# Performance work log

Hardware: AMD Instinct MI355X
Metric: run time of the kernel (lower is better)

The kernel has to match this reference:

```python
import jax, jax.numpy as jnp
import numpy as np

HID = 256   # hidden_dim
P = 16      # pool_size
EPS = 1e-5


def _ln(x, g, b):
    m = x.mean(-1, keepdims=True)
    v = x.var(-1, keepdims=True)
    return (x - m) * jax.lax.rsqrt(v + EPS) * g + b


def setup_inputs() -> dict:
    key = jax.random.key(0)
    ks = jax.random.split(key, 12)
    B, Cf, H, W = 8, 512, 64, 64
    Cg = Cf // 2
    Co = Cf // 2
    s = 0.02
    d = {}
    d['e_f'] = jax.random.normal(ks[0], (B, Cf, H, W), jnp.float32)
    d['e_g'] = jax.random.normal(ks[1], (B, Cg, H, W), jnp.float32)
    d['l_feat'] = jax.random.normal(ks[2], (B, 768, 20), jnp.float32)
    d['l_mask'] = jnp.ones((B, 20, 1), jnp.float32)
    d['ln_f_g'] = jnp.ones((Cf,), jnp.float32)
    d['ln_f_b'] = jnp.zeros((Cf,), jnp.float32)
    d['ln_g_g'] = jnp.ones((Cg,), jnp.float32)
    d['ln_g_b'] = jnp.zeros((Cg,), jnp.float32)
    d['wq'] = jax.random.normal(ks[3], (Cf, HID), jnp.float32) * s
    d['bq'] = jnp.zeros((HID,), jnp.float32)
    d['wk'] = jax.random.normal(ks[4], (Cg, HID), jnp.float32) * s
    d['bk'] = jnp.zeros((HID,), jnp.float32)
    d['wv'] = jax.random.normal(ks[5], (Cg, HID), jnp.float32) * s
    d['bv'] = jnp.zeros((HID,), jnp.float32)
    d['wo'] = jax.random.normal(ks[6], (HID, HID), jnp.float32) * s
    d['bo'] = jnp.zeros((HID,), jnp.float32)
    d['dw_k'] = jax.random.normal(ks[7], (HID, 1, 3, 3), jnp.float32) * s  # depthwise kernel (OIHW, I=1)
    d['efp_w'] = jax.random.normal(ks[8], (HID, Cf), jnp.float32) * s     # 1x1 conv v_channels->hidden
    d['efp_b'] = jnp.zeros((HID,), jnp.float32)
    d['outc_w'] = jax.random.normal(ks[9], (Co, HID), jnp.float32) * s    # 1x1 conv hidden->out
    d['outc_b'] = jnp.zeros((Co,), jnp.float32)
    d['bn_g'] = jnp.ones((Co,), jnp.float32)
    d['bn_b'] = jnp.zeros((Co,), jnp.float32)
    d['bn_m'] = jnp.zeros((Co,), jnp.float32)
    d['bn_v'] = jnp.ones((Co,), jnp.float32)
    return d


def reference(e_f, e_g, l_feat, l_mask, ln_f_g, ln_f_b, ln_g_g, ln_g_b,
              wq, bq, wk, bk, wv, bv, wo, bo, dw_k, efp_w, efp_b,
              outc_w, outc_b, bn_g, bn_b, bn_m, bn_v):
    B, Cf, H, W = e_f.shape
    # Q = w_qi(LN(e_f))                                  (B, HW, HID)
    q = _ln(e_f.transpose(0, 2, 3, 1), ln_f_g, ln_f_b).reshape(B, H * W, Cf) @ wq + bq
    # K/V projections from LN(e_g)
    g = _ln(e_g.transpose(0, 2, 3, 1), ln_g_g, ln_g_b).reshape(B, H * W, -1)
    k = (g @ wk + bk).reshape(B, H, W, HID)
    v = (g @ wv + bv).reshape(B, H, W, HID)
    # 16x16 max/avg pooling -> (B, Hp*Wp, HID)
    k = jnp.max(k.reshape(B, H // P, P, W // P, P, HID), axis=(2, 4)).reshape(B, -1, HID)
    v = jnp.mean(v.reshape(B, H // P, P, W // P, P, HID), axis=(2, 4)).reshape(B, -1, HID)
    # pooled attention
    attn = jax.nn.softmax(jnp.einsum('bqd,bkd->bqk', q, k) * (HID ** -0.5), axis=-1)
    a_i = jnp.einsum('bqk,bkd->bqd', attn, v)  # (B, HW, HID)
    # depthwise 3x3 conv on Q (NCHW)
    q_nchw = q.reshape(B, H, W, HID).transpose(0, 3, 1, 2)
    dw = jax.lax.conv_general_dilated(q_nchw, dw_k, (1, 1), [(1, 1), (1, 1)],
                                      feature_group_count=HID)
    combined = dw + a_i.reshape(B, H, W, HID).transpose(0, 3, 1, 2)
    comb = combined.transpose(0, 2, 3, 1).reshape(B, H * W, HID) @ wo + bo
    comb = comb.reshape(B, H, W, HID).transpose(0, 3, 1, 2)
    # 1x1 proj of e_f, elementwise gate
    efp = jnp.einsum('bchw,oc->bohw', e_f, efp_w) + efp_b[None, :, None, None]
    e_a = efp * comb
    # out: 1x1 conv + BN (inference) + ReLU (dropout inactive in eval)
    out = jnp.einsum('bchw,oc->bohw', e_a, outc_w) + outc_b[None, :, None, None]
    scale = (bn_g * jax.lax.rsqrt(bn_v + EPS))[None, :, None, None]
    out = (out - bn_m[None, :, None, None]) * scale + bn_b[None, :, None, None]
    return jax.nn.relu(out)
```

## Files before the change

### kernel.cpp

```cpp
#include <hip/hip_runtime.h>
#include <math.h>

#define EPS 1e-5f

typedef __attribute__((ext_vector_type(8))) short bf16x8;
typedef __attribute__((ext_vector_type(4))) float f32x4;

__device__ __forceinline__ unsigned short f2bf(float f) {
    unsigned int u = __float_as_uint(f);
    u += 0x7fff + ((u >> 16) & 1);
    return (unsigned short)(u >> 16);
}
__device__ __forceinline__ float bf2f(unsigned short h) {
    return __uint_as_float(((unsigned int)h) << 16);
}
__device__ __forceinline__ float lof(unsigned int u) {
    return __uint_as_float(u << 16);
}
__device__ __forceinline__ float hif(unsigned int u) {
    return __uint_as_float(u & 0xffff0000u);
}
__device__ __forceinline__ void async16(void* lds, const void* g) {
    __builtin_amdgcn_global_load_lds(
        (const __attribute__((address_space(1))) unsigned int*)g,
        (__attribute__((address_space(3))) unsigned int*)lds, 16, 0, 0);
}

__global__ __launch_bounds__(256) void trans_prep(
    const float* __restrict__ ef, const float* __restrict__ eg,
    unsigned short* __restrict__ ef_bf, unsigned short* __restrict__ eg_bf,
    float* __restrict__ pf, float* __restrict__ pfq,
    float* __restrict__ pg, float* __restrict__ pgq,
    const float* __restrict__ lnfg, const float* __restrict__ lnfb,
    const float* __restrict__ wq, const float* __restrict__ bq,
    const float* __restrict__ efpw, const float* __restrict__ efpb,
    const float* __restrict__ lngg, const float* __restrict__ lngb,
    const float* __restrict__ wk, const float* __restrict__ bk,
    const float* __restrict__ wv, const float* __restrict__ bv,
    const float* __restrict__ wo, const float* __restrict__ outcw,
    const float* __restrict__ outcb, const float* __restrict__ bng,
    const float* __restrict__ bnb, const float* __restrict__ bnm,
    const float* __restrict__ bnv, const float* __restrict__ dwk,
    unsigned short* __restrict__ Wb1t, unsigned short* __restrict__ Wb2t,
    unsigned short* __restrict__ Wot, unsigned short* __restrict__ Woc,
    float* __restrict__ dwt,
    float* __restrict__ cs1, float* __restrict__ cst1,
    float* __restrict__ cs2, float* __restrict__ cst2,
    float* __restrict__ scv, float* __restrict__ shv)
{
    __shared__ float tile[64][65];
    __shared__ float psum[4][64], pss[4][64];
    int id = blockIdx.x;
    int t = threadIdx.x;
    if (id < 3072) {
        const float* src; unsigned short* dst; float* ps; float* pq;
        int C, cblk, b, p0;
        if (id < 2048) {
            src = ef; dst = ef_bf; ps = pf; pq = pfq; C = 512;
            b = id >> 8; cblk = (id >> 5) & 7; p0 = (id & 31) * 128;
        } else {
            id -= 2048;
            src = eg; dst = eg_bf; ps = pg; pq = pgq; C = 256;
            b = id >> 7; cblk = (id >> 5) & 3; p0 = (id & 31) * 128;
        }
        int c0 = cblk * 64;
        const float* s = src + ((size_t)b * C + c0) * 4096 + p0;
        int cr = t >> 4, p4 = (t & 15) * 4;
        int lane = t & 63, grp = t >> 6;
        int pr = t >> 3, c8 = (t & 7) * 8;

        float4 r1[4], r2[4];
#pragma unroll
        for (int i = 0; i < 4; i++)
            r1[i] = *(const float4*)(s + (size_t)(i * 16 + cr) * 4096 + p4);
#pragma unroll
        for (int i = 0; i < 4; i++)
            r2[i] = *(const float4*)(s + (size_t)(i * 16 + cr) * 4096 + 64 + p4);

#pragma unroll
        for (int half = 0; half < 2; half++) {
#pragma unroll
            for (int i = 0; i < 4; i++) {
                float4 v = half ? r2[i] : r1[i];
                int c = i * 16 + cr;
                tile[c][p4 + 0] = v.x; tile[c][p4 + 1] = v.y;
                tile[c][p4 + 2] = v.z; tile[c][p4 + 3] = v.w;
            }
            __syncthreads();

            int pbase = p0 + half * 64;
            unsigned short* d = dst + ((size_t)(b * 4096 + pbase)) * C + c0;
#pragma unroll
            for (int i = 0; i < 2; i++) {
                int p = i * 32 + pr;
                uint4 pk;
                pk.x = (unsigned)f2bf(tile[c8 + 0][p]) | ((unsigned)f2bf(tile[c8 + 1][p]) << 16);
                pk.y = (unsigned)f2bf(tile[c8 + 2][p]) | ((unsigned)f2bf(tile[c8 + 3][p]) << 16);
                pk.z = (unsigned)f2bf(tile[c8 + 4][p]) | ((unsigned)f2bf(tile[c8 + 5][p]) << 16);
                pk.w = (unsigned)f2bf(tile[c8 + 6][p]) | ((unsigned)f2bf(tile[c8 + 7][p]) << 16);
                *(uint4*)(d + (size_t)p * C + c8) = pk;
            }

            float sm = 0.f, sq = 0.f;
#pragma unroll
            for (int j = 0; j < 16; j++) {
                float v = tile[grp * 16 + j][lane];
                sm += v; sq += v * v;
            }
            psum[grp][lane] = sm; pss[grp][lane] = sq;
            __syncthreads();
            if (t < 64) {
                float fs = psum[0][t] + psum[1][t] + psum[2][t] + psum[3][t];
                float fq = pss[0][t] + pss[1][t] + pss[2][t] + pss[3][t];
                ps[cblk * 32768 + b * 4096 + pbase + t] = fs;
                pq[cblk * 32768 + b * 4096 + pbase + t] = fq;
            }
            if (half == 0) __syncthreads();
        }
    } else {
        int id2 = id - 3072;
        float* red1 = (float*)psum;
        float* red2 = (float*)pss;
        if (id2 < 64) {
            const float* src; unsigned short* dst; const float* scale;
            int K, k0, n0;
            if (id2 < 32) {
                src = wq; dst = Wb1t; scale = lnfg; K = 512;
                k0 = (id2 >> 2) * 64; n0 = (id2 & 3) * 64;
            } else if (id2 < 48) {
                int j = id2 - 32;
                src = wk; dst = Wb2t; scale = lngg; K = 256;
                k0 = (j >> 2) * 64; n0 = (j & 3) * 64;
            } else {
                int j = id2 - 48;
                src = wo; dst = Wot; scale = nullptr; K = 256;
                k0 = (j >> 2) * 64; n0 = (j & 3) * 64;
            }
            int rr = t >> 6, cc = t & 63;
#pragma unroll
            for (int i = 0; i < 16; i++) {
                int r = i * 4 + rr;
                tile[r][cc] = src[(size_t)(k0 + r) * 256 + n0 + cc];
            }
            __syncthreads();
            int nn = t >> 3, k8 = (t & 7) * 8;
#pragma unroll
            for (int i = 0; i < 2; i++) {
                int n = i * 32 + nn;
                float v[8];
#pragma unroll
                for (int j = 0; j < 8; j++) {
                    float s = scale ? scale[k0 + k8 + j] : 1.f;
                    v[j] = s * tile[k8 + j][n];
                }
                uint4 pk;
                pk.x = (unsigned)f2bf(v[0]) | ((unsigned)f2bf(v[1]) << 16);
                pk.y = (unsigned)f2bf(v[2]) | ((unsigned)f2bf(v[3]) << 16);
                pk.z = (unsigned)f2bf(v[4]) | ((unsigned)f2bf(v[5]) << 16);
                pk.w = (unsigned)f2bf(v[6]) | ((unsigned)f2bf(v[7]) << 16);
                *(uint4*)(dst + (size_t)(n0 + n) * K + k0 + k8) = pk;
            }
        } else if (id2 < 192) {
            int j = (id2 - 64) * 1024 + t * 4;
            float4 v = *(const float4*)(efpw + j);
            uint2 pk;
            pk.x = (unsigned)f2bf(v.x) | ((unsigned)f2bf(v.y) << 16);
            pk.y = (unsigned)f2bf(v.z) | ((unsigned)f2bf(v.w) << 16);
            *(uint2*)(Wb1t + 131072 + j) = pk;
        } else if (id2 < 256) {
            int j = (id2 - 192) * 1024 + t * 4;
            float4 v = *(const float4*)(outcw + j);
            uint2 pk;
            pk.x = (unsigned)f2bf(v.x) | ((unsigned)f2bf(v.y) << 16);
            pk.y = (unsigned)f2bf(v.z) | ((unsigned)f2bf(v.w) << 16);
            *(uint2*)(Woc + j) = pk;
        } else if (id2 == 256) {
#pragma unroll
            for (int tap = 0; tap < 9; tap++)
                dwt[tap * 256 + t] = dwk[t * 9 + tap];
        } else if (id2 < 265) {
            int n0 = (id2 - 257) * 32;
            int nl = t & 31, kq = t >> 5;
            float cs = 0.f, ct = 0.f;
#pragma unroll 4
            for (int kk = 0; kk < 64; kk++) {
                int k = kq * 64 + kk;
                float w = wq[k * 256 + n0 + nl];
                cs += lnfg[k] * w; ct += lnfb[k] * w;
            }
            red1[kq * 32 + nl] = cs; red2[kq * 32 + nl] = ct;
            __syncthreads();
            if (t < 32) {
                float s = 0.f, c2 = 0.f;
#pragma unroll
                for (int q = 0; q < 8; q++) { s += red1[q * 32 + t]; c2 += red2[q * 32 + t]; }
                int n = n0 + t;
                cs1[n] = s; cst1[n] = c2 + bq[n];
                cs1[256 + n] = 0.f; cst1[256 + n] = efpb[n];
            }
        } else if (id2 < 273) {
            int n0 = (id2 - 265) * 32;
            int nl = t & 31, kq = t >> 5;
            float cs = 0.f, ct = 0.f;
#pragma unroll 4
            for (int kk = 0; kk < 32; kk++) {
                int k = kq * 32 + kk;
                float w = wk[k * 256 + n0 + nl];
                cs += lngg[k] * w; ct += lngb[k] * w;
            }
            red1[kq * 32 + nl] = cs; red2[kq * 32 + nl] = ct;
            __syncthreads();
            if (t < 32) {
                float s = 0.f, c2 = 0.f;
#pragma unroll
                for (int q = 0; q < 8; q++) { s += red1[q * 32 + t]; c2 += red2[q * 32 + t]; }
                int n = n0 + t;
                cs2[n] = s; cst2[n] = c2 + bk[n];
            }
        } else if (id2 < 281) {
            int n0 = (id2 - 273) * 32;
            int nl = t & 31, kq = t >> 5;
            float cs = 0.f, ct = 0.f;
#pragma unroll 4
            for (int kk = 0; kk < 32; kk++) {
                int k = kq * 32 + kk;
                float w = wv[k * 256 + n0 + nl];
                cs += lngg[k] * w; ct += lngb[k] * w;
            }
            red1[kq * 32 + nl] = cs; red2[kq * 32 + nl] = ct;
            __syncthreads();
            if (t < 32) {
                float s = 0.f, c2 = 0.f;
#pragma unroll
                for (int q = 0; q < 8; q++) { s += red1[q * 32 + t]; c2 += red2[q * 32 + t]; }
                int n = n0 + t;
                cs2[256 + n] = s; cst2[256 + n] = c2 + bv[n];
            }
        } else {
            int n = t;
            float s = bng[n] * rsqrtf(bnv[n] + EPS);
            scv[n] = s;
            shv[n] = (outcb[n] - bnm[n]) * s + bnb[n];
        }
    }
}

template<int K>
__device__ __forceinline__ void mfma_core(
    const unsigned short* __restrict__ A, const unsigned short* __restrict__ Bt,
    int m0, int n0, unsigned short* As, unsigned short* Bs, f32x4 acc[4][4])
{
    const int tid = threadIdx.x;
    const int wave = tid >> 6, lane = tid & 63;
    const int wm = (wave & 1) * 64, wn = (wave >> 1) * 64;
#pragma unroll
    for (int i = 0; i < 4; i++)
#pragma unroll
        for (int j = 0; j < 4; j++) acc[i][j] = (f32x4){0.f, 0.f, 0.f, 0.f};

    const int srow = wave * 32 + (lane >> 3);
    const int sg = (lane & 7) ^ ((lane >> 3) & 7);
    const unsigned short* ga = A + (size_t)(m0 + srow) * K + sg * 8;
    const unsigned short* gb = Bt + (size_t)(n0 + srow) * K + sg * 8;

    for (int k0 = 0; k0 < K; k0 += 64) {
#pragma unroll
        for (int t = 0; t < 4; t++) {
            async16(As + (wave * 32 + t * 8) * 64, ga + (size_t)t * 8 * K + k0);
            async16(Bs + (wave * 32 + t * 8) * 64, gb + (size_t)t * 8 * K + k0);
        }
        __syncthreads();
#pragma unroll
        for (int ks = 0; ks < 2; ks++) {
            bf16x8 af[4], bfr[4];
            int kb = ks * 4 + (lane >> 4);
            int slot = (kb ^ (lane & 7)) * 8;
#pragma unroll
            for (int i = 0; i < 4; i++) {
                int m = wm + i * 16 + (lane & 15);
                af[i] = *(const bf16x8*)&As[m * 64 + slot];
                int n = wn + i * 16 + (lane & 15);
                bfr[i] = *(const bf16x8*)&Bs[n * 64 + slot];
            }
#pragma unroll
            for (int i = 0; i < 4; i++)
#pragma unroll
                for (int j = 0; j < 4; j++)
                    acc[i][j] = __builtin_amdgcn_mfma_f32_16x16x32_bf16(
                        af[i], bfr[j], acc[i][j], 0, 0, 0);
        }
        __syncthreads();
    }
}

__global__ __launch_bounds__(256, 2) void gemm_proj(
    const unsigned short* __restrict__ ef_bf, const unsigned short* __restrict__ Wb1t,
    const float* __restrict__ cs1, const float* __restrict__ cst1,
    const float* __restrict__ pf, const float* __restrict__ pfq,
    unsigned short* __restrict__ qbuf, unsigned short* __restrict__ efpbuf,
    const unsigned short* __restrict__ eg_bf, const unsigned short* __restrict__ Wb2t,
    const float* __restrict__ cs2, const float* __restrict__ cst2,
    const float* __restrict__ pg, const float* __restrict__ pgq,
    float* __restrict__ mg, float* __restrict__ rg,
    unsigned short* __restrict__ kfull)
{
    __shared__ unsigned short As[128 * 64];
    __shared__ unsigned short Bs[256 * 64];
    __shared__ float sstat[256];
    const int tid = threadIdx.x;
    const int wave = tid >> 6, lane = tid & 63;
    const int bid = blockIdx.x;

    if (bid < 512) {
        const int m0 = (bid >> 1) * 128, n0 = (bid & 1) * 256;
        const int wm = (wave & 1) * 64, wn = (wave >> 1) * 128;
        f32x4 acc[4][8];

        if (tid < 128) {
            int gm = m0 + tid;
            float s = 0.f, q = 0.f;
#pragma unroll
            for (int i = 0; i < 8; i++) { s += pf[i * 32768 + gm]; q += pfq[i * 32768 + gm]; }
            float m = s * (1.f / 512.f);
            sstat[tid] = m;
            sstat[128 + tid] = rsqrtf(q * (1.f / 512.f) - m * m + EPS);
        }

#pragma unroll
        for (int i = 0; i < 4; i++)
#pragma unroll
            for (int j = 0; j < 8; j++) acc[i][j] = (f32x4){0.f, 0.f, 0.f, 0.f};

        const int srow = lane >> 3;
        const int sg = (lane & 7) ^ (srow & 7);
        const unsigned short* ga = ef_bf + (size_t)(m0 + wave * 32 + srow) * 512 + sg * 8;
        const unsigned short* gb = Wb1t + (size_t)(n0 + wave * 64 + srow) * 512 + sg * 8;

        for (int k0 = 0; k0 < 512; k0 += 64) {
#pragma unroll
            for (int t = 0; t < 4; t++)
                async16(As + (wave * 32 + t * 8) * 64, ga + (size_t)t * 8 * 512 + k0);
#pragma unroll
            for (int t = 0; t < 8; t++)
                async16(Bs + (wave * 64 + t * 8) * 64, gb + (size_t)t * 8 * 512 + k0);
            __syncthreads();
#pragma unroll
            for (int ks = 0; ks < 2; ks++) {
                bf16x8 af[4], bfr[8];
                int kb = ks * 4 + (lane >> 4);
                int slot = (kb ^ (lane & 7)) * 8;
#pragma unroll
                for (int i = 0; i < 4; i++)
                    af[i] = *(const bf16x8*)&As[(wm + i * 16 + (lane & 15)) * 64 + slot];
#pragma unroll
                for (int j = 0; j < 8; j++)
                    bfr[j] = *(const bf16x8*)&Bs[(wn + j * 16 + (lane & 15)) * 64 + slot];
#pragma unroll
                for (int i = 0; i < 4; i++)
#pragma unroll
                    for (int j = 0; j < 8; j++)
                        acc[i][j] = __builtin_amdgcn_mfma_f32_16x16x32_bf16(
                            af[i], bfr[j], acc[i][j], 0, 0, 0);
            }
            __syncthreads();
        }

        bool isq = (n0 == 0);
#pragma unroll
        for (int i = 0; i < 4; i++) {
#pragma unroll
            for (int r = 0; r < 4; r++) {
                int lm = wm + i * 16 + ((lane >> 4) * 4) + r;
                int gm = m0 + lm;
                float mean = sstat[lm], rs = sstat[128 + lm];
#pragma unroll
                for (int j = 0; j < 8; j++) {
                    int nn = wn + j * 16 + (lane & 15);
                    float v = acc[i][j][r];
                    if (isq) {
                        int n = nn;
                        float o = rs * (v - mean * cs1[n]) + cst1[n];
                        qbuf[(size_t)gm * 256 + nn] = f2bf(o);
                    } else {
                        int n = nn + 256;
                        efpbuf[(size_t)gm * 256 + nn] = f2bf(v + cst1[n]);
                    }
                }
            }
        }
    } else {
        const int j2 = bid - 512;
        const int m0 = (j2 >> 1) * 128, n0 = (j2 & 1) * 128;
        f32x4 acc[4][4];

        if (tid < 128) {
            int gm = m0 + tid;
            float s = 0.f, q = 0.f;
#pragma unroll
            for (int i = 0; i < 4; i++) { s += pg[i * 32768 + gm]; q += pgq[i * 32768 + gm]; }
            float m = s * (1.f / 256.f);
            float r = rsqrtf(q * (1.f / 256.f) - m * m + EPS);
            sstat[tid] = m; sstat[128 + tid] = r;
            if (n0 == 0) { mg[gm] = m; rg[gm] = r; }
        }

        mfma_core<256>(eg_bf, Wb2t, m0, n0, As, Bs, acc);
        int wm = (wave & 1) * 64, wn = (wave >> 1) * 64;
#pragma unroll
        for (int i = 0; i < 4; i++) {
#pragma unroll
            for (int r = 0; r < 4; r++) {
                int lm = wm + i * 16 + ((lane >> 4) * 4) + r;
                int gm = m0 + lm;
                float mean = sstat[lm], rs = sstat[128 + lm];
#pragma unroll
                for (int j = 0; j < 4; j++) {
                    int n = n0 + wn + j * 16 + (lane & 15);
                    float o = rs * (acc[i][j][r] - mean * cs2[n]) + cst2[n];
                    kfull[(size_t)gm * 256 + n] = f2bf(o);
                }
            }
        }
    }
}

__global__ __launch_bounds__(256) void pool_phase(
    const unsigned short* __restrict__ kfull, const float* __restrict__ eg,
    const float* __restrict__ rg, const float* __restrict__ mg,
    unsigned short* __restrict__ kpb, float* __restrict__ s1,
    float* __restrict__ s0)
{
    __shared__ float smem[4352];
    int id = blockIdx.x;
    int t = threadIdx.x;
    if (id < 128) {
        int b = id >> 4, cell = id & 15;
        int hp = cell >> 2, wp = cell & 3;
        int g8 = t & 31, rr = t >> 5;
        float kmx[8];
#pragma unroll
        for (int j = 0; j < 8; j++) kmx[j] = -3.402823466e38f;
#pragma unroll
        for (int rsub = 0; rsub < 2; rsub++) {
            int r = rr * 2 + rsub;
            int prow = (hp * 16 + r) * 64 + wp * 16;
            for (int cl = 0; cl < 16; cl++) {
                size_t basei = ((size_t)(b * 4096 + prow + cl)) * 256 + g8 * 8;
                uint4 kv = *(const uint4*)(kfull + basei);
                kmx[0] = fmaxf(kmx[0], lof(kv.x)); kmx[1] = fmaxf(kmx[1], hif(kv.x));
                kmx[2] = fmaxf(kmx[2], lof(kv.y)); kmx[3] = fmaxf(kmx[3], hif(kv.y));
                kmx[4] = fmaxf(kmx[4], lof(kv.z)); kmx[5] = fmaxf(kmx[5], hif(kv.z));
                kmx[6] = fmaxf(kmx[6], lof(kv.w)); kmx[7] = fmaxf(kmx[7], hif(kv.w));
            }
        }
#pragma unroll
        for (int j = 0; j < 8; j++) smem[rr * 256 + g8 * 8 + j] = kmx[j];
        __syncthreads();
        float m = smem[t];
#pragma unroll
        for (int r2 = 1; r2 < 8; r2++) m = fmaxf(m, smem[r2 * 256 + t]);
        kpb[(size_t)(b * 16 + cell) * 256 + t] = f2bf(m);
    } else {
        int id2 = id - 128;
        int b = id2 >> 6, hp = (id2 >> 4) & 3, cgrp = id2 & 15;
        int rr = t >> 4, cq = t & 15, cx = cq >> 2;
        int p = (hp * 16 + rr) * 64 + cq * 4;
        float4 w4 = *(const float4*)&rg[b * 4096 + p];
        float part[16];
        const float* egb = eg + ((size_t)b * 256 + cgrp * 16) * 4096 + p;
#pragma unroll
        for (int cc = 0; cc < 16; cc++) {
            float4 v4 = *(const float4*)(egb + (size_t)cc * 4096);
            part[cc] = w4.x * v4.x + w4.y * v4.y + w4.z * v4.z + w4.w * v4.w;
        }
#pragma unroll
        for (int cc = 0; cc < 16; cc++) smem[t * 16 + cc] = part[cc];
        if (cgrp == 0) {
            float4 m4 = *(const float4*)&mg[b * 4096 + p];
            smem[4096 + t] = w4.x * m4.x + w4.y * m4.y + w4.z * m4.z + w4.w * m4.w;
        }
        __syncthreads();
        if (t < 64) {
            int cx2 = t >> 4, cc = t & 15;
            float sacc = 0.f;
#pragma unroll
            for (int rr2 = 0; rr2 < 16; rr2++)
#pragma unroll
                for (int dq = 0; dq < 4; dq++)
                    sacc += smem[(rr2 * 16 + cx2 * 4 + dq) * 16 + cc];
            s1[((size_t)(b * 16 + hp * 4 + cx2)) * 256 + cgrp * 16 + cc] = sacc;
        }
        if (cgrp == 0 && t < 4) {
            float sacc = 0.f;
#pragma unroll
            for (int rr2 = 0; rr2 < 16; rr2++)
#pragma unroll
                for (int dq = 0; dq < 4; dq++)
                    sacc += smem[4096 + rr2 * 16 + t * 4 + dq];
            s0[b * 16 + hp * 4 + t] = sacc;
        }
    }
}

__global__ __launch_bounds__(256) void vpool_gemm(
    const float* __restrict__ s1, const float* __restrict__ s0,
    const float* __restrict__ lngg, const float* __restrict__ wv,
    const float* __restrict__ cs2, const float* __restrict__ cst2,
    float* __restrict__ vp)
{
    int cell = blockIdx.x;
    int n = threadIdx.x;
    const float* s1r = s1 + (size_t)cell * 256;
    float acc = 0.f;
    for (int c = 0; c < 256; c++)
        acc = fmaf(lngg[c] * s1r[c], wv[c * 256 + n], acc);
    vp[(size_t)cell * 256 + n] = acc * (1.f / 256.f)
        - (s0[cell] * (1.f / 256.f)) * cs2[256 + n] + cst2[256 + n];
}

__global__ __launch_bounds__(256) void combined_dw(
    const unsigned short* __restrict__ qbuf, const unsigned short* __restrict__ kpb,
    const float* __restrict__ vp, const float* __restrict__ dwt,
    unsigned short* __restrict__ combined)
{
    __shared__ float attns[256];
    int wave = threadIdx.x >> 6, lane = threadIdx.x & 63;
    int id = blockIdx.x;
    int b = id & 7, seg = id >> 3;
    int pidx0 = seg * 16;

    if (wave == 0) {
        int fr = lane & 15, quad = lane >> 4;
        const unsigned short* qrow = qbuf + (size_t)(b * 4096 + pidx0 + fr) * 256 + quad * 8;
        const unsigned short* krow = kpb + (size_t)(b * 16 + fr) * 256 + quad * 8;
        f32x4 sacc = {0.f, 0.f, 0.f, 0.f};
#pragma unroll
        for (int ks = 0; ks < 8; ks++) {
            bf16x8 af = *(const bf16x8*)(qrow + ks * 32);
            bf16x8 bf_ = *(const bf16x8*)(krow + ks * 32);
            sacc = __builtin_amdgcn_mfma_f32_16x16x32_bf16(af, bf_, sacc, 0, 0, 0);
        }
#pragma unroll
        for (int r = 0; r < 4; r++) {
            float s = sacc[r] * 0.0625f;
            float mx = s;
#pragma unroll
            for (int off = 8; off >= 1; off >>= 1) mx = fmaxf(mx, __shfl_xor(mx, off));
            float e = __expf(s - mx);
            float sum = e;
#pragma unroll
            for (int off = 8; off >= 1; off >>= 1) sum += __shfl_xor(sum, off);
            attns[(quad * 4 + r) * 16 + fr] = e / sum;
        }
    }
    __syncthreads();

    int pidx = pidx0 + wave * 4;
    int h = pidx >> 6, w0 = pidx & 63;
    int o4 = lane * 4;

    float4 kreg[9];
#pragma unroll
    for (int tap = 0; tap < 9; tap++)
        kreg[tap] = *(const float4*)&dwt[tap * 256 + o4];

    float4 acc[4];
#pragma unroll
    for (int i = 0; i < 4; i++) acc[i] = (float4){0.f, 0.f, 0.f, 0.f};

    const float* arow = attns + (wave * 4) * 16;
#pragma unroll
    for (int c = 0; c < 16; c++) {
        float4 v = *(const float4*)&vp[(size_t)(b * 16 + c) * 256 + o4];
#pragma unroll
        for (int i = 0; i < 4; i++) {
            float a = arow[i * 16 + c];
            acc[i].x = fmaf(a, v.x, acc[i].x); acc[i].y = fmaf(a, v.y, acc[i].y);
            acc[i].z = fmaf(a, v.z, acc[i].z); acc[i].w = fmaf(a, v.w, acc[i].w);
        }
    }
#pragma unroll
    for (int dy = 0; dy < 3; dy++) {
        int hh = h + dy - 1;
        if (hh < 0 || hh > 63) continue;
        const unsigned short* qr = qbuf + ((size_t)(b * 4096 + hh * 64)) * 256;
        float4 ft[6];
#pragma unroll
        for (int c = 0; c < 6; c++) {
            int xx = w0 - 1 + c;
            if (xx < 0 || xx > 63) {
                ft[c] = (float4){0.f, 0.f, 0.f, 0.f};
            } else {
                uint2 qa = *(const uint2*)(qr + (size_t)xx * 256 + o4);
                ft[c] = (float4){lof(qa.x), hif(qa.x), lof(qa.y), hif(qa.y)};
            }
        }
#pragma unroll
        for (int dx = 0; dx < 3; dx++) {
            float4 kk = kreg[dy * 3 + dx];
#pragma unroll
            for (int i = 0; i < 4; i++) {
                float4 qv = ft[i + dx];
                acc[i].x = fmaf(qv.x, kk.x, acc[i].x);
                acc[i].y = fmaf(qv.y, kk.y, acc[i].y);
                acc[i].z = fmaf(qv.z, kk.z, acc[i].z);
                acc[i].w = fmaf(qv.w, kk.w, acc[i].w);
            }
        }
    }
#pragma unroll
    for (int i = 0; i < 4; i++) {
        uint2 pk;
        pk.x = (unsigned)f2bf(acc[i].x) | ((unsigned)f2bf(acc[i].y) << 16);
        pk.y = (unsigned)f2bf(acc[i].z) | ((unsigned)f2bf(acc[i].w) << 16);
        *(uint2*)(combined + ((size_t)(b * 4096 + pidx + i)) * 256 + o4) = pk;
    }
}

__global__ __launch_bounds__(256) void gemm34_mfma(
    const unsigned short* __restrict__ comb, const unsigned short* __restrict__ Wot,
    const float* __restrict__ bo, const unsigned short* __restrict__ efp,
    const unsigned short* __restrict__ Woc,
    const float* __restrict__ scv, const float* __restrict__ shv,
    float* __restrict__ outp)
{
    __shared__ unsigned short As[64 * 64];
    __shared__ unsigned short Bs[256 * 64];
    __shared__ unsigned short eat[64 * 256];
    const int tid = threadIdx.x;
    const int wave = tid >> 6, lane = tid & 63;
    const int m0 = blockIdx.x * 64;

    const int srow = lane >> 3;
    const int sg = (lane & 7) ^ (srow & 7);

    f32x4 acc[4][4];
#pragma unroll
    for (int i = 0; i < 4; i++)
#pragma unroll
        for (int j = 0; j < 4; j++) acc[i][j] = (f32x4){0.f, 0.f, 0.f, 0.f};

    const unsigned short* ga = comb + (size_t)(m0 + wave * 16 + srow) * 256 + sg * 8;
    const unsigned short* gb = Wot + (size_t)(wave * 64 + srow) * 256 + sg * 8;

    for (int k0 = 0; k0 < 256; k0 += 64) {
#pragma unroll
        for (int t = 0; t < 2; t++)
            async16(As + (wave * 16 + t * 8) * 64, ga + (size_t)t * 8 * 256 + k0);
#pragma unroll
        for (int t = 0; t < 8; t++)
            async16(Bs + (wave * 64 + t * 8) * 64, gb + (size_t)t * 8 * 256 + k0);
        __syncthreads();
#pragma unroll
        for (int ks = 0; ks < 2; ks++) {
            bf16x8 af[4], bfr[4];
            int kb = ks * 4 + (lane >> 4);
            int slot = (kb ^ (lane & 7)) * 8;
#pragma unroll
            for (int i = 0; i < 4; i++) {
                af[i]  = *(const bf16x8*)&As[(i * 16 + (lane & 15)) * 64 + slot];
                bfr[i] = *(const bf16x8*)&Bs[(wave * 64 + i * 16 + (lane & 15)) * 64 + slot];
            }
#pragma unroll
            for (int i = 0; i < 4; i++)
#pragma unroll
                for (int j = 0; j < 4; j++)
                    acc[i][j] = __builtin_amdgcn_mfma_f32_16x16x32_bf16(
                        af[i], bfr[j], acc[i][j], 0, 0, 0);
        }
        __syncthreads();
    }

    float bo4[4];
#pragma unroll
    for (int j = 0; j < 4; j++) bo4[j] = bo[wave * 64 + j * 16 + (lane & 15)];
#pragma unroll
    for (int i = 0; i < 4; i++) {
#pragma unroll
        for (int r = 0; r < 4; r++) {
            int pos = i * 16 + ((lane >> 4) * 4) + r;
#pragma unroll
            for (int j = 0; j < 4; j++) {
                int n = wave * 64 + j * 16 + (lane & 15);
                float o = (acc[i][j][r] + bo4[j])
                          * bf2f(efp[(size_t)(m0 + pos) * 256 + n]);
                int o8 = j * 2 + ((lane >> 3) & 1);
                int slot = o8 ^ (pos & 7);
                eat[pos * 256 + wave * 64 + slot * 8 + (lane & 7)] = f2bf(o);
            }
        }
    }

    f32x4 acc2[4][4];
#pragma unroll
    for (int i = 0; i < 4; i++)
#pragma unroll
        for (int j = 0; j < 4; j++) acc2[i][j] = (f32x4){0.f, 0.f, 0.f, 0.f};

    const unsigned short* gw = Woc + (size_t)(wave * 64 + srow) * 256 + sg * 8;
    for (int k0 = 0; k0 < 256; k0 += 64) {
#pragma unroll
        for (int t = 0; t < 8; t++)
            async16(Bs + (wave * 64 + t * 8) * 64, gw + (size_t)t * 8 * 256 + k0);
        __syncthreads();
        int kc = k0 >> 6;
#pragma unroll
        for (int ks = 0; ks < 2; ks++) {
            bf16x8 af2[4], bf2_[4];
            int kb = ks * 4 + (lane >> 4);
            int slot = (kb ^ (lane & 7)) * 8;
#pragma unroll
            for (int i = 0; i < 4; i++) {
                af2[i]  = *(const bf16x8*)&Bs[(wave * 64 + i * 16 + (lane & 15)) * 64 + slot];
                bf2_[i] = *(const bf16x8*)&eat[(i * 16 + (lane & 15)) * 256 + kc * 64 + slot];
            }
#pragma unroll
            for (int i = 0; i < 4; i++)
#pragma unroll
                for (int j = 0; j < 4; j++)
                    acc2[i][j] = __builtin_amdgcn_mfma_f32_16x16x32_bf16(
                        af2[i], bf2_[j], acc2[i][j], 0, 0, 0);
        }
        __syncthreads();
    }

#pragma unroll
    for (int i = 0; i < 4; i++) {
#pragma unroll
        for (int r = 0; r < 4; r++) {
            int co = wave * 64 + i * 16 + ((lane >> 4) * 4) + r;
            float s = scv[co], hh = shv[co];
#pragma unroll
            for (int j = 0; j < 4; j++) {
                int p = m0 + j * 16 + (lane & 15);
                float o = fmaxf(fmaf(acc2[i][j][r], s, hh), 0.f);
                outp[((size_t)(p >> 12)) * 1048576 + (size_t)co * 4096 + (p & 4095)] = o;
            }
        }
    }
}

extern "C" void kernel_launch(void* const* d_in, const int* in_sizes, int n_in,
                              void* d_out, int out_size, void* d_ws, size_t ws_size,
                              hipStream_t stream)
{
    const float* e_f   = (const float*)d_in[0];
    const float* e_g   = (const float*)d_in[1];
    const float* lnfg  = (const float*)d_in[4];
    const float* lnfb  = (const float*)d_in[5];
    const float* lngg  = (const float*)d_in[6];
    const float* lngb  = (const float*)d_in[7];
    const float* wq    = (const float*)d_in[8];
    const float* bq    = (const float*)d_in[9];
    const float* wk    = (const float*)d_in[10];
    const float* bk    = (const float*)d_in[11];
    const float* wv    = (const float*)d_in[12];
    const float* bv    = (const float*)d_in[13];
    const float* wo    = (const float*)d_in[14];
    const float* bo    = (const float*)d_in[15];
    const float* dwk   = (const float*)d_in[16];
    const float* efpw  = (const float*)d_in[17];
    const float* efpb  = (const float*)d_in[18];
    const float* outcw = (const float*)d_in[19];
    const float* outcb = (const float*)d_in[20];
    const float* bng   = (const float*)d_in[21];
    const float* bnb   = (const float*)d_in[22];
    const float* bnm   = (const float*)d_in[23];
    const float* bnv   = (const float*)d_in[24];
    float* outp = (float*)d_out;

    char* base = (char*)d_ws;
    auto alloc = [&](size_t bytes) -> char* {
        char* r = base; base += (bytes + 255) & ~(size_t)255; return r;
    };
    float* pf    = (float*)alloc(8 * 32768 * 4);
    float* pfq   = (float*)alloc(8 * 32768 * 4);
    float* pg    = (float*)alloc(4 * 32768 * 4);
    float* pgq   = (float*)alloc(4 * 32768 * 4);
    float* mg    = (float*)alloc(32768 * 4);
    float* rg    = (float*)alloc(32768 * 4);
    float* cs1   = (float*)alloc(512 * 4);
    float* cst1  = (float*)alloc(512 * 4);
    float* cs2   = (float*)alloc(512 * 4);
    float* cst2  = (float*)alloc(512 * 4);
    float* scv   = (float*)alloc(256 * 4);
    float* shv   = (float*)alloc(256 * 4);
    float* dwt   = (float*)alloc(9 * 256 * 4);
    unsigned short* Wb1t = (unsigned short*)alloc(262144 * 2);
    unsigned short* Wb2t = (unsigned short*)alloc(65536 * 2);
    unsigned short* Wot  = (unsigned short*)alloc(65536 * 2);
    unsigned short* Woc  = (unsigned short*)alloc(65536 * 2);
    unsigned short* ef_bf = (unsigned short*)alloc((size_t)32768 * 512 * 2);
    unsigned short* eg_bf = (unsigned short*)alloc((size_t)32768 * 256 * 2);
    unsigned short* qbuf  = (unsigned short*)alloc((size_t)32768 * 256 * 2);
    unsigned short* efpbuf = (unsigned short*)alloc((size_t)32768 * 256 * 2);
    unsigned short* kfull = (unsigned short*)alloc((size_t)32768 * 256 * 2);
    unsigned short* kpb  = (unsigned short*)alloc(128 * 256 * 2);
    float* vp    = (float*)alloc(128 * 256 * 4);
    float* s1    = (float*)alloc(128 * 256 * 4);
    float* s0    = (float*)alloc(128 * 4);

    trans_prep<<<3354, 256, 0, stream>>>(
        e_f, e_g, ef_bf, eg_bf, pf, pfq, pg, pgq,
        lnfg, lnfb, wq, bq, efpw, efpb, lngg, lngb, wk, bk, wv, bv, wo,
        outcw, outcb, bng, bnb, bnm, bnv, dwk,
        Wb1t, Wb2t, Wot, Woc, dwt, cs1, cst1, cs2, cst2, scv, shv);
    gemm_proj<<<1024, 256, 0, stream>>>(
        ef_bf, Wb1t, cs1, cst1, pf, pfq, qbuf, efpbuf,
        eg_bf, Wb2t, cs2, cst2, pg, pgq, mg, rg, kfull);
    pool_phase<<<640, 256, 0, stream>>>(kfull, e_g, rg, mg, kpb, s1, s0);
    vpool_gemm<<<128, 256, 0, stream>>>(s1, s0, lngg, wv, cs2, cst2, vp);
    combined_dw<<<2048, 256, 0, stream>>>(qbuf, kpb, vp, dwt, kfull);
    gemm34_mfma<<<512, 256, 0, stream>>>(kfull, Wot, bo, efpbuf,
                                         Woc, scv, shv, outp);
}
```

Baseline: 289.0 us.

## Fold V-pool statistics into projection GEMM launch and merge K-pool with V GEMM

```diff
diff --git a/kernel.cpp b/kernel.cpp
--- a/kernel.cpp
+++ b/kernel.cpp
@@ -301,8 +301,9 @@
     const unsigned short* __restrict__ eg_bf, const unsigned short* __restrict__ Wb2t,
     const float* __restrict__ cs2, const float* __restrict__ cst2,
     const float* __restrict__ pg, const float* __restrict__ pgq,
-    float* __restrict__ mg, float* __restrict__ rg,
-    unsigned short* __restrict__ kfull)
+    unsigned short* __restrict__ kfull,
+    const float* __restrict__ eg, float* __restrict__ s1,
+    float* __restrict__ s0)
 {
     __shared__ unsigned short As[128 * 64];
     __shared__ unsigned short Bs[256 * 64];
@@ -388,7 +389,7 @@
                 }
             }
         }
-    } else {
+    } else if (bid < 1024) {
         const int j2 = bid - 512;
         const int m0 = (j2 >> 1) * 128, n0 = (j2 & 1) * 128;
         f32x4 acc[4][4];
@@ -401,7 +402,6 @@
             float m = s * (1.f / 256.f);
             float r = rsqrtf(q * (1.f / 256.f) - m * m + EPS);
             sstat[tid] = m; sstat[128 + tid] = r;
-            if (n0 == 0) { mg[gm] = m; rg[gm] = r; }
         }
 
         mfma_core<256>(eg_bf, Wb2t, m0, n0, As, Bs, acc);
@@ -421,16 +421,67 @@
                 }
             }
         }
-    }
-}
-
-__global__ __launch_bounds__(256) void pool_phase(
-    const unsigned short* __restrict__ kfull, const float* __restrict__ eg,
-    const float* __restrict__ rg, const float* __restrict__ mg,
-    unsigned short* __restrict__ kpb, float* __restrict__ s1,
-    float* __restrict__ s0)
+    } else {
+        float* smem = (float*)Bs;
+        const int id3 = bid - 1024;
+        int b = id3 >> 6, hp = (id3 >> 4) & 3, cgrp = id3 & 15;
+        int rr = tid >> 4, cq = tid & 15;
+        int p = (hp * 16 + rr) * 64 + cq * 4;
+
+        float w[4], m[4];
+#pragma unroll
+        for (int d = 0; d < 4; d++) {
+            int gp = b * 4096 + p + d;
+            float s = 0.f, q = 0.f;
+#pragma unroll
+            for (int i = 0; i < 4; i++) { s += pg[i * 32768 + gp]; q += pgq[i * 32768 + gp]; }
+            float mean = s * (1.f / 256.f);
+            m[d] = mean;
+            w[d] = rsqrtf(q * (1.f / 256.f) - mean * mean + EPS);
+        }
+
+        float part[16];
+        const float* egb = eg + ((size_t)b * 256 + cgrp * 16) * 4096 + p;
+#pragma unroll
+        for (int cc = 0; cc < 16; cc++) {
+            float4 v4 = *(const float4*)(egb + (size_t)cc * 4096);
+            part[cc] = w[0] * v4.x + w[1] * v4.y + w[2] * v4.z + w[3] * v4.w;
+        }
+#pragma unroll
+        for (int cc = 0; cc < 16; cc++) smem[tid * 16 + cc] = part[cc];
+        if (cgrp == 0)
+            smem[4096 + tid] = w[0] * m[0] + w[1] * m[1] + w[2] * m[2] + w[3] * m[3];
+        __syncthreads();
+        if (tid < 64) {
+            int cx2 = tid >> 4, cc = tid & 15;
+            float sacc = 0.f;
+#pragma unroll
+            for (int rr2 = 0; rr2 < 16; rr2++)
+#pragma unroll
+                for (int dq = 0; dq < 4; dq++)
+                    sacc += smem[(rr2 * 16 + cx2 * 4 + dq) * 16 + cc];
+            s1[((size_t)(b * 16 + hp * 4 + cx2)) * 256 + cgrp * 16 + cc] = sacc;
+        }
+        if (cgrp == 0 && tid < 4) {
+            float sacc = 0.f;
+#pragma unroll
+            for (int rr2 = 0; rr2 < 16; rr2++)
+#pragma unroll
+                for (int dq = 0; dq < 4; dq++)
+                    sacc += smem[4096 + rr2 * 16 + tid * 4 + dq];
+            s0[b * 16 + hp * 4 + tid] = sacc;
+        }
+    }
+}
+
+__global__ __launch_bounds__(256) void pool_vp(
+    const unsigned short* __restrict__ kfull, unsigned short* __restrict__ kpb,
+    const float* __restrict__ s1, const float* __restrict__ s0,
+    const float* __restrict__ lngg, const float* __restrict__ wv,
+    const float* __restrict__ cs2, const float* __restrict__ cst2,
+    float* __restrict__ vp)
 {
-    __shared__ float smem[4352];
+    __shared__ float smem[2048];
     int id = blockIdx.x;
     int t = threadIdx.x;
     if (id < 128) {
@@ -461,61 +512,15 @@
         for (int r2 = 1; r2 < 8; r2++) m = fmaxf(m, smem[r2 * 256 + t]);
         kpb[(size_t)(b * 16 + cell) * 256 + t] = f2bf(m);
     } else {
-        int id2 = id - 128;
-        int b = id2 >> 6, hp = (id2 >> 4) & 3, cgrp = id2 & 15;
-        int rr = t >> 4, cq = t & 15, cx = cq >> 2;
-        int p = (hp * 16 + rr) * 64 + cq * 4;
-        float4 w4 = *(const float4*)&rg[b * 4096 + p];
-        float part[16];
-        const float* egb = eg + ((size_t)b * 256 + cgrp * 16) * 4096 + p;
-#pragma unroll
-        for (int cc = 0; cc < 16; cc++) {
-            float4 v4 = *(const float4*)(egb + (size_t)cc * 4096);
-            part[cc] = w4.x * v4.x + w4.y * v4.y + w4.z * v4.z + w4.w * v4.w;
-        }
-#pragma unroll
-        for (int cc = 0; cc < 16; cc++) smem[t * 16 + cc] = part[cc];
-        if (cgrp == 0) {
-            float4 m4 = *(const float4*)&mg[b * 4096 + p];
-            smem[4096 + t] = w4.x * m4.x + w4.y * m4.y + w4.z * m4.z + w4.w * m4.w;
-        }
-        __syncthreads();
-        if (t < 64) {
-            int cx2 = t >> 4, cc = t & 15;
-            float sacc = 0.f;
-#pragma unroll
-            for (int rr2 = 0; rr2 < 16; rr2++)
-#pragma unroll
-                for (int dq = 0; dq < 4; dq++)
-                    sacc += smem[(rr2 * 16 + cx2 * 4 + dq) * 16 + cc];
-            s1[((size_t)(b * 16 + hp * 4 + cx2)) * 256 + cgrp * 16 + cc] = sacc;
-        }
-        if (cgrp == 0 && t < 4) {
-            float sacc = 0.f;
-#pragma unroll
-            for (int rr2 = 0; rr2 < 16; rr2++)
-#pragma unroll
-                for (int dq = 0; dq < 4; dq++)
-                    sacc += smem[4096 + rr2 * 16 + t * 4 + dq];
-            s0[b * 16 + hp * 4 + t] = sacc;
-        }
-    }
-}
-
-__global__ __launch_bounds__(256) void vpool_gemm(
-    const float* __restrict__ s1, const float* __restrict__ s0,
-    const float* __restrict__ lngg, const float* __restrict__ wv,
-    const float* __restrict__ cs2, const float* __restrict__ cst2,
-    float* __restrict__ vp)
-{
-    int cell = blockIdx.x;
-    int n = threadIdx.x;
-    const float* s1r = s1 + (size_t)cell * 256;
-    float acc = 0.f;
-    for (int c = 0; c < 256; c++)
-        acc = fmaf(lngg[c] * s1r[c], wv[c * 256 + n], acc);
-    vp[(size_t)cell * 256 + n] = acc * (1.f / 256.f)
-        - (s0[cell] * (1.f / 256.f)) * cs2[256 + n] + cst2[256 + n];
+        int cell = id - 128;
+        int n = t;
+        const float* s1r = s1 + (size_t)cell * 256;
+        float acc = 0.f;
+        for (int c = 0; c < 256; c++)
+            acc = fmaf(lngg[c] * s1r[c], wv[c * 256 + n], acc);
+        vp[(size_t)cell * 256 + n] = acc * (1.f / 256.f)
+            - (s0[cell] * (1.f / 256.f)) * cs2[256 + n] + cst2[256 + n];
+    }
 }
 
 __global__ __launch_bounds__(256) void combined_dw(
@@ -777,8 +782,6 @@
     float* pfq   = (float*)alloc(8 * 32768 * 4);
     float* pg    = (float*)alloc(4 * 32768 * 4);
     float* pgq   = (float*)alloc(4 * 32768 * 4);
-    float* mg    = (float*)alloc(32768 * 4);
-    float* rg    = (float*)alloc(32768 * 4);
     float* cs1   = (float*)alloc(512 * 4);
     float* cst1  = (float*)alloc(512 * 4);
     float* cs2   = (float*)alloc(512 * 4);
@@ -805,11 +808,11 @@
         lnfg, lnfb, wq, bq, efpw, efpb, lngg, lngb, wk, bk, wv, bv, wo,
         outcw, outcb, bng, bnb, bnm, bnv, dwk,
         Wb1t, Wb2t, Wot, Woc, dwt, cs1, cst1, cs2, cst2, scv, shv);
-    gemm_proj<<<1024, 256, 0, stream>>>(
+    gemm_proj<<<1536, 256, 0, stream>>>(
         ef_bf, Wb1t, cs1, cst1, pf, pfq, qbuf, efpbuf,
-        eg_bf, Wb2t, cs2, cst2, pg, pgq, mg, rg, kfull);
-    pool_phase<<<640, 256, 0, stream>>>(kfull, e_g, rg, mg, kpb, s1, s0);
-    vpool_gemm<<<128, 256, 0, stream>>>(s1, s0, lngg, wv, cs2, cst2, vp);
+        eg_bf, Wb2t, cs2, cst2, pg, pgq, kfull,
+        e_g, s1, s0);
+    pool_vp<<<256, 256, 0, stream>>>(kfull, kpb, s1, s0, lngg, wv, cs2, cst2, vp);
     combined_dw<<<2048, 256, 0, stream>>>(qbuf, kpb, vp, dwt, kfull);
     gemm34_mfma<<<512, 256, 0, stream>>>(kfull, Wot, bo, efpbuf,
                                          Woc, scv, shv, outp);
```

After: 287.4 us. Within noise of the previous version (-0.6%).
